# Performance work log

Hardware: AMD Instinct MI355X
Metric: run time of the kernel (lower is better)

## Reference

```python
import jax, jax.numpy as jnp
from jax import lax
import numpy as np

QMAX = 127.0  # int8 symmetric quant range


def setup_inputs() -> dict:
    key = jax.random.key(0)
    k1, k2, k3, k4 = jax.random.split(key, 4)
    B, S, D_in, D_out = 4, 2048, 4096, 4096
    x = jax.random.normal(k1, (B, S, D_in), dtype=jnp.float32)
    # pre-quantized per-channel weights [output_size, input_size]
    weight_q = jax.random.randint(k2, (D_out, D_in), -127, 128, dtype=jnp.int32).astype(jnp.int8)
    weight_scale = (jax.random.uniform(k3, (D_out,), dtype=jnp.float32) + 0.5) * 0.01
    bias = jax.random.normal(k4, (D_out,), dtype=jnp.float32) * 0.02
    return {"x": x, "weight_q": weight_q, "weight_scale": weight_scale, "bias": bias}


def reference(x, weight_q, weight_scale, bias):
    """Dynamic per-token int8 activation quant + int8 matmul + dequant + bias.

    x: [..., D_in] float32; weight_q: [D_out, D_in] int8;
    weight_scale: [D_out]; bias: [D_out]. Returns [..., D_out] float32.
    """
    orig_shape = x.shape
    x2 = x.reshape(-1, orig_shape[-1])  # [T, D_in]
    # dynamic per-token symmetric quantization
    amax = jnp.max(jnp.abs(x2), axis=-1, keepdims=True)  # [T, 1]
    x_scale = jnp.maximum(amax, 1e-8) / QMAX
    x_q = jnp.clip(jnp.round(x2 / x_scale), -128.0, QMAX).astype(jnp.int8)
    acc = lax.dot_general(x_q, weight_q, (((1,), (1,)), ((), ())),
                          preferred_element_type=jnp.int32)  # [T, D_out]
    out = acc.astype(jnp.float32) * x_scale * weight_scale[None, :]
    out = out.reshape(*orig_shape[:-1], out.shape[-1]) + bias
    return out
```

## Files before the change

kernel.cpp:

```cpp
#include <hip/hip_runtime.h>

typedef __attribute__((ext_vector_type(4))) int int4v;

__global__ __launch_bounds__(256) void pack_w_kernel(const int* __restrict__ w32,
                                                     int* __restrict__ w8,
                                                     long n4) {
    long i = (long)blockIdx.x * 256 + threadIdx.x;
    if (i >= n4) return;
    int4v v = ((const int4v*)w32)[i];
    w8[i] = (v[0] & 0xFF) | ((v[1] & 0xFF) << 8) |
            ((v[2] & 0xFF) << 16) | ((v[3] & 0xFF) << 24);
}

template <int NCHUNK>
__global__ __launch_bounds__(256) void quant_kernel(const float* __restrict__ x,
                                                    signed char* __restrict__ xq,
                                                    float* __restrict__ xs,
                                                    int K) {
    const int t = blockIdx.x;
    const int tid = threadIdx.x;
    const float4* row = (const float4*)(x + (size_t)t * K);

    float4 v[NCHUNK];
    float amax = 0.0f;
    #pragma unroll
    for (int i = 0; i < NCHUNK; ++i) {
        float4 f = row[i * 256 + tid];
        v[i] = f;
        amax = fmaxf(amax, fmaxf(fmaxf(fabsf(f.x), fabsf(f.y)),
                                 fmaxf(fabsf(f.z), fabsf(f.w))));
    }
    #pragma unroll
    for (int off = 32; off >= 1; off >>= 1)
        amax = fmaxf(amax, __shfl_xor(amax, off, 64));
    __shared__ float red[4];
    if ((tid & 63) == 0) red[tid >> 6] = amax;
    __syncthreads();
    amax = fmaxf(fmaxf(red[0], red[1]), fmaxf(red[2], red[3]));

    const float scale = fmaxf(amax, 1e-8f) / 127.0f;
    if (tid == 0) xs[t] = scale;
    const float inv = 1.0f / scale;

    int* orow = (int*)(xq + (size_t)t * K);
    #pragma unroll
    for (int i = 0; i < NCHUNK; ++i) {
        float4 f = v[i];
        int q0 = (int)fminf(fmaxf(rintf(f.x * inv), -128.0f), 127.0f);
        int q1 = (int)fminf(fmaxf(rintf(f.y * inv), -128.0f), 127.0f);
        int q2 = (int)fminf(fmaxf(rintf(f.z * inv), -128.0f), 127.0f);
        int q3 = (int)fminf(fmaxf(rintf(f.w * inv), -128.0f), 127.0f);
        orow[i * 256 + tid] =
            (q0 & 0xFF) | ((q1 & 0xFF) << 8) | ((q2 & 0xFF) << 16) | ((q3 & 0xFF) << 24);
    }
}

#define BM 256
#define BN 256
#define BKB 128

#define MFMA_I8 __builtin_amdgcn_mfma_i32_16x16x64_i8

#define BARRIER()                       \
    do {                                \
        __builtin_amdgcn_s_barrier();   \
        asm volatile("" ::: "memory");  \
    } while (0)

#define LGKM0() asm volatile("s_waitcnt lgkmcnt(0)" ::: "memory")
#define VMCNT4() asm volatile("s_waitcnt vmcnt(4)" ::: "memory")

#define STAGE_HALF(GL, LB, ROWOFF, KK)                                        \
    do {                                                                      \
        __builtin_amdgcn_global_load_lds(                                     \
            (const __attribute__((address_space(1))) void*)(                  \
                (GL) + (size_t)(ROWOFF) * K + (KK)),                          \
            (__attribute__((address_space(3))) void*)((LB) + (ROWOFF) * BKB), \
            16, 0, 0);                                                        \
        __builtin_amdgcn_global_load_lds(                                     \
            (const __attribute__((address_space(1))) void*)(                  \
                (GL) + (size_t)((ROWOFF) + 64) * K + (KK)),                   \
            (__attribute__((address_space(3))) void*)(                        \
                (LB) + ((ROWOFF) + 64) * BKB),                                \
            16, 0, 0);                                                        \
    } while (0)

#define LDA4(RP, MOFF)                                                     \
    do {                                                                   \
        af[0][0] = *(const int4v*)((RP) + ((MOFF) + 0) * 2048 + sw0);      \
        af[0][1] = *(const int4v*)((RP) + ((MOFF) + 0) * 2048 + sw1);      \
        af[1][0] = *(const int4v*)((RP) + ((MOFF) + 1) * 2048 + sw0);      \
        af[1][1] = *(const int4v*)((RP) + ((MOFF) + 1) * 2048 + sw1);      \
        af[2][0] = *(const int4v*)((RP) + ((MOFF) + 2) * 2048 + sw0);      \
        af[2][1] = *(const int4v*)((RP) + ((MOFF) + 2) * 2048 + sw1);      \
        af[3][0] = *(const int4v*)((RP) + ((MOFF) + 3) * 2048 + sw0);      \
        af[3][1] = *(const int4v*)((RP) + ((MOFF) + 3) * 2048 + sw1);      \
    } while (0)

#define LDB2M(RP, NB)                                                      \
    do {                                                                   \
        bf[(NB) + 0][0] = *(const int4v*)((RP) + ((NB) + 0) * 2048 + sw0); \
        bf[(NB) + 0][1] = *(const int4v*)((RP) + ((NB) + 0) * 2048 + sw1); \
        bf[(NB) + 1][0] = *(const int4v*)((RP) + ((NB) + 1) * 2048 + sw0); \
        bf[(NB) + 1][1] = *(const int4v*)((RP) + ((NB) + 1) * 2048 + sw1); \
    } while (0)

#define QUAD(MB, NB)                                                          \
    do {                                                                      \
        _Pragma("unroll") for (int m_ = 0; m_ < 4; ++m_) {                    \
            _Pragma("unroll") for (int n_ = 0; n_ < 2; ++n_) {                \
                acc[(MB) + m_][(NB) + n_] = MFMA_I8(                          \
                    af[m_][0], bf[(NB) + n_][0], acc[(MB) + m_][(NB) + n_],   \
                    0, 0, 0);                                                 \
                acc[(MB) + m_][(NB) + n_] = MFMA_I8(                          \
                    af[m_][1], bf[(NB) + n_][1], acc[(MB) + m_][(NB) + n_],   \
                    0, 0, 0);                                                 \
            }                                                                 \
        }                                                                     \
    } while (0)

__global__ __launch_bounds__(512, 2) void gemm_i8_kernel(
    const signed char* __restrict__ A,
    const signed char* __restrict__ B,
    const float* __restrict__ xs,
    const float* __restrict__ wsc,
    const float* __restrict__ bias,
    float* __restrict__ C,
    int M, int N, int K) {
    __shared__ __align__(16) signed char lds[2][2][BM * BKB];

    const int tid = threadIdx.x;
    const int lane = tid & 63;
    const int wv = tid >> 6;
    const int wrow = wv >> 2;
    const int wcol = wv & 3;
    const int fr = lane & 15;
    const int q = lane >> 4;

    const int bm = blockIdx.y * BM;
    const int bn = blockIdx.x * BN;

    const int srow = wv * 8 + (lane >> 3);
    const int scol = ((lane & 7) ^ ((lane >> 3) & 7)) << 4;
    const signed char* gA = A + (size_t)(bm + srow) * K + scol;
    const signed char* gB = B + (size_t)(bn + srow) * K + scol;

    signed char* wA0 = &lds[0][0][0] + wv * 1024;
    signed char* wA1 = &lds[1][0][0] + wv * 1024;
    signed char* wB0 = &lds[0][1][0] + wv * 1024;
    signed char* wB1 = &lds[1][1][0] + wv * 1024;

    const int rowA = (wrow * 128 + fr) * BKB;
    const int rowB = (wcol * 64 + fr) * BKB;
    const int sw0 = ((0 + q) ^ (fr & 7)) << 4;
    const int sw1 = ((4 + q) ^ (fr & 7)) << 4;
    const signed char* rA0 = &lds[0][0][0] + rowA;
    const signed char* rA1 = &lds[1][0][0] + rowA;
    const signed char* rB0 = &lds[0][1][0] + rowB;
    const signed char* rB1 = &lds[1][1][0] + rowB;

    int4v acc[8][4];
    const int4v zero = {0, 0, 0, 0};
    #pragma unroll
    for (int m = 0; m < 8; ++m)
        #pragma unroll
        for (int n = 0; n < 4; ++n) acc[m][n] = zero;
    int4v af[4][2], bf[4][2];

    STAGE_HALF(gA, wA0, 0, 0);
    STAGE_HALF(gA, wA0, 128, 0);
    STAGE_HALF(gB, wB0, 0, 0);
    STAGE_HALF(gB, wB0, 128, 0);
    STAGE_HALF(gB, wB1, 0, (size_t)BKB);
    STAGE_HALF(gB, wB1, 128, (size_t)BKB);
    VMCNT4();
    BARRIER();

    const int NT = K / BKB;
    for (int i = 0; i < NT / 2; ++i) {
        const size_t kk1 = (size_t)(2 * i + 1) * BKB;
        int t2 = 2 * i + 2; if (t2 >= NT) t2 -= NT;
        int t3 = 2 * i + 3; if (t3 >= NT) t3 -= NT;
        const size_t kk2 = (size_t)t2 * BKB;
        const size_t kk3 = (size_t)t3 * BKB;

        LDA4(rA0, 0);
        LDB2M(rB0, 0);
        STAGE_HALF(gA, wA1, 0, kk1);
        BARRIER();
        LGKM0();
        __builtin_amdgcn_s_setprio(1);
        QUAD(0, 0);
        __builtin_amdgcn_s_setprio(0);
        BARRIER();

        LDB2M(rB0, 2);
        STAGE_HALF(gA, wA1, 128, kk1);
        BARRIER();
        LGKM0();
        __builtin_amdgcn_s_setprio(1);
        QUAD(0, 2);
        __builtin_amdgcn_s_setprio(0);
        BARRIER();

        LDA4(rA0, 4);
        STAGE_HALF(gB, wB0, 0, kk2);
        BARRIER();
        LGKM0();
        __builtin_amdgcn_s_setprio(1);
        QUAD(4, 2);
        __builtin_amdgcn_s_setprio(0);
        BARRIER();

        STAGE_HALF(gB, wB0, 128, kk2);
        VMCNT4();
        BARRIER();
        __builtin_amdgcn_s_setprio(1);
        QUAD(4, 0);
        __builtin_amdgcn_s_setprio(0);
        BARRIER();

        LDA4(rA1, 0);
        LDB2M(rB1, 0);
        STAGE_HALF(gA, wA0, 0, kk2);
        BARRIER();
        LGKM0();
        __builtin_amdgcn_s_setprio(1);
        QUAD(0, 0);
        __builtin_amdgcn_s_setprio(0);
        BARRIER();

        LDB2M(rB1, 2);
        STAGE_HALF(gA, wA0, 128, kk2);
        BARRIER();
        LGKM0();
        __builtin_amdgcn_s_setprio(1);
        QUAD(0, 2);
        __builtin_amdgcn_s_setprio(0);
        BARRIER();

        LDA4(rA1, 4);
        STAGE_HALF(gB, wB1, 0, kk3);
        BARRIER();
        LGKM0();
        __builtin_amdgcn_s_setprio(1);
        QUAD(4, 2);
        __builtin_amdgcn_s_setprio(0);
        BARRIER();

        STAGE_HALF(gB, wB1, 128, kk3);
        VMCNT4();
        BARRIER();
        __builtin_amdgcn_s_setprio(1);
        QUAD(4, 0);
        __builtin_amdgcn_s_setprio(0);
        BARRIER();
    }

    asm volatile("s_waitcnt vmcnt(0)" ::: "memory");

    const int cb = bn + wcol * 64;
    float wv4[4], bv4[4];
    #pragma unroll
    for (int n = 0; n < 4; ++n) {
        wv4[n] = wsc[cb + n * 16 + fr];
        bv4[n] = bias[cb + n * 16 + fr];
    }
    #pragma unroll
    for (int m = 0; m < 8; ++m) {
        #pragma unroll
        for (int r = 0; r < 4; ++r) {
            const int row = bm + wrow * 128 + m * 16 + q * 4 + r;
            const float s = xs[row];
            float* crow = C + (size_t)row * N + cb + fr;
            #pragma unroll
            for (int n = 0; n < 4; ++n)
                crow[n * 16] = (float)acc[m][n][r] * s * wv4[n] + bv4[n];
        }
    }
}

extern "C" void kernel_launch(void* const* d_in, const int* in_sizes, int n_in,
                              void* d_out, int out_size, void* d_ws, size_t ws_size,
                              hipStream_t stream) {
    const float* x = (const float*)d_in[0];
    const int* wq32 = (const int*)d_in[1];
    const float* wscale = (const float*)d_in[2];
    const float* bias = (const float*)d_in[3];
    float* out = (float*)d_out;

    const int d_out_dim = in_sizes[2];
    const int d_in_dim = in_sizes[1] / d_out_dim;
    const int T = in_sizes[0] / d_in_dim;

    const size_t wbytes = (size_t)d_out_dim * d_in_dim;
    signed char* w8 = (signed char*)d_ws;
    signed char* xq = (signed char*)d_ws + wbytes;
    float* xscl = (float*)((char*)d_ws + wbytes + (size_t)T * d_in_dim);

    const long n4 = (long)d_out_dim * d_in_dim / 4;
    pack_w_kernel<<<(int)((n4 + 255) / 256), 256, 0, stream>>>(wq32, (int*)w8, n4);

    if (d_in_dim == 4096) {
        quant_kernel<4><<<T, 256, 0, stream>>>(x, xq, xscl, d_in_dim);
    } else {
        quant_kernel<8><<<T, 256, 0, stream>>>(x, xq, xscl, d_in_dim);
    }

    dim3 grid(d_out_dim / BN, T / BM);
    gemm_i8_kernel<<<grid, 512, 0, stream>>>(xq, w8, xscl, wscale, bias, out,
                                             T, d_out_dim, d_in_dim);
}
```

Before: 383.0 us.

## Switch int8 GEMM to 32x32x32 MFMA with reworked fragment loads and epilogue

Replaces the 16x16x64 int8 MFMA with the 32x32x32 variant, so each wave computes its 128x64 tile as 4x2 blocks of 32x32 instead of 8x4 blocks of 16x16. LDS fragment loads, swizzle offsets, the per-phase MFMA schedule and the output row mapping are all rewritten to match the new lane layout. The larger MFMA reduces fragment reloads per FLOP and the number of instructions issued. In exchange, A fragments are now reloaded in every phase, and the epilogue writes wider-strided rows.

```diff
diff --git a/kernel.cpp b/kernel.cpp
--- a/kernel.cpp
+++ b/kernel.cpp
@@ -1,6 +1,7 @@
 #include <hip/hip_runtime.h>
 
 typedef __attribute__((ext_vector_type(4))) int int4v;
+typedef __attribute__((ext_vector_type(16))) int int16v;
 
 __global__ __launch_bounds__(256) void pack_w_kernel(const int* __restrict__ w32,
                                                      int* __restrict__ w8,
@@ -59,7 +60,7 @@
 #define BN 256
 #define BKB 128
 
-#define MFMA_I8 __builtin_amdgcn_mfma_i32_16x16x64_i8
+#define MFMA32 __builtin_amdgcn_mfma_i32_32x32x32_i8
 
 #define BARRIER()                       \
     do {                                \
@@ -85,36 +86,31 @@
             16, 0, 0);                                                        \
     } while (0)
 
-#define LDA4(RP, MOFF)                                                     \
+#define LDA_PAIR(RP, MB, C0, C1)                                           \
     do {                                                                   \
-        af[0][0] = *(const int4v*)((RP) + ((MOFF) + 0) * 2048 + sw0);      \
-        af[0][1] = *(const int4v*)((RP) + ((MOFF) + 0) * 2048 + sw1);      \
-        af[1][0] = *(const int4v*)((RP) + ((MOFF) + 1) * 2048 + sw0);      \
-        af[1][1] = *(const int4v*)((RP) + ((MOFF) + 1) * 2048 + sw1);      \
-        af[2][0] = *(const int4v*)((RP) + ((MOFF) + 2) * 2048 + sw0);      \
-        af[2][1] = *(const int4v*)((RP) + ((MOFF) + 2) * 2048 + sw1);      \
-        af[3][0] = *(const int4v*)((RP) + ((MOFF) + 3) * 2048 + sw0);      \
-        af[3][1] = *(const int4v*)((RP) + ((MOFF) + 3) * 2048 + sw1);      \
-    } while (0)
-
-#define LDB2M(RP, NB)                                                      \
+        af[0][0] = *(const int4v*)((RP) + ((MB) + 0) * 4096 + (C0));       \
+        af[0][1] = *(const int4v*)((RP) + ((MB) + 0) * 4096 + (C1));       \
+        af[1][0] = *(const int4v*)((RP) + ((MB) + 1) * 4096 + (C0));       \
+        af[1][1] = *(const int4v*)((RP) + ((MB) + 1) * 4096 + (C1));       \
+    } while (0)
+
+#define LDB_PAIR(RP, KP, C0, C1)                                           \
     do {                                                                   \
-        bf[(NB) + 0][0] = *(const int4v*)((RP) + ((NB) + 0) * 2048 + sw0); \
-        bf[(NB) + 0][1] = *(const int4v*)((RP) + ((NB) + 0) * 2048 + sw1); \
-        bf[(NB) + 1][0] = *(const int4v*)((RP) + ((NB) + 1) * 2048 + sw0); \
-        bf[(NB) + 1][1] = *(const int4v*)((RP) + ((NB) + 1) * 2048 + sw1); \
-    } while (0)
-
-#define QUAD(MB, NB)                                                          \
+        bf[0][(KP)*2 + 0] = *(const int4v*)((RP) + 0 * 4096 + (C0));       \
+        bf[0][(KP)*2 + 1] = *(const int4v*)((RP) + 0 * 4096 + (C1));       \
+        bf[1][(KP)*2 + 0] = *(const int4v*)((RP) + 1 * 4096 + (C0));       \
+        bf[1][(KP)*2 + 1] = *(const int4v*)((RP) + 1 * 4096 + (C1));       \
+    } while (0)
+
+#define QUAD32(MB, KP)                                                        \
     do {                                                                      \
-        _Pragma("unroll") for (int m_ = 0; m_ < 4; ++m_) {                    \
-            _Pragma("unroll") for (int n_ = 0; n_ < 2; ++n_) {                \
-                acc[(MB) + m_][(NB) + n_] = MFMA_I8(                          \
-                    af[m_][0], bf[(NB) + n_][0], acc[(MB) + m_][(NB) + n_],   \
-                    0, 0, 0);                                                 \
-                acc[(MB) + m_][(NB) + n_] = MFMA_I8(                          \
-                    af[m_][1], bf[(NB) + n_][1], acc[(MB) + m_][(NB) + n_],   \
-                    0, 0, 0);                                                 \
+        _Pragma("unroll") for (int kl_ = 0; kl_ < 2; ++kl_) {                 \
+            _Pragma("unroll") for (int m_ = 0; m_ < 2; ++m_) {                \
+                _Pragma("unroll") for (int n_ = 0; n_ < 2; ++n_) {            \
+                    acc[(MB) + m_][n_] = MFMA32(af[m_][kl_],                  \
+                                                bf[n_][(KP)*2 + kl_],         \
+                                                acc[(MB) + m_][n_], 0, 0, 0); \
+                }                                                             \
             }                                                                 \
         }                                                                     \
     } while (0)
@@ -134,8 +130,8 @@
     const int wv = tid >> 6;
     const int wrow = wv >> 2;
     const int wcol = wv & 3;
-    const int fr = lane & 15;
-    const int q = lane >> 4;
+    const int fr32 = lane & 31;
+    const int kb = lane >> 5;
 
     const int bm = blockIdx.y * BM;
     const int bn = blockIdx.x * BN;
@@ -150,22 +146,27 @@
     signed char* wB0 = &lds[0][1][0] + wv * 1024;
     signed char* wB1 = &lds[1][1][0] + wv * 1024;
 
-    const int rowA = (wrow * 128 + fr) * BKB;
-    const int rowB = (wcol * 64 + fr) * BKB;
-    const int sw0 = ((0 + q) ^ (fr & 7)) << 4;
-    const int sw1 = ((4 + q) ^ (fr & 7)) << 4;
+    const int rowA = (wrow * 128 + fr32) * BKB;
+    const int rowB = (wcol * 64 + fr32) * BKB;
+    const int l7 = lane & 7;
+    const int c0 = ((0 + kb) ^ l7) << 4;
+    const int c1 = ((2 + kb) ^ l7) << 4;
+    const int c2 = ((4 + kb) ^ l7) << 4;
+    const int c3 = ((6 + kb) ^ l7) << 4;
     const signed char* rA0 = &lds[0][0][0] + rowA;
     const signed char* rA1 = &lds[1][0][0] + rowA;
     const signed char* rB0 = &lds[0][1][0] + rowB;
     const signed char* rB1 = &lds[1][1][0] + rowB;
 
-    int4v acc[8][4];
-    const int4v zero = {0, 0, 0, 0};
-    #pragma unroll
-    for (int m = 0; m < 8; ++m)
+    int16v acc[4][2];
+    #pragma unroll
+    for (int m = 0; m < 4; ++m)
         #pragma unroll
-        for (int n = 0; n < 4; ++n) acc[m][n] = zero;
-    int4v af[4][2], bf[4][2];
+        for (int n = 0; n < 2; ++n)
+            #pragma unroll
+            for (int e = 0; e < 16; ++e) acc[m][n][e] = 0;
+    int4v af[2][2];
+    int4v bf[2][4];
 
     STAGE_HALF(gA, wA0, 0, 0);
     STAGE_HALF(gA, wA0, 128, 0);
@@ -184,75 +185,81 @@
         const size_t kk2 = (size_t)t2 * BKB;
         const size_t kk3 = (size_t)t3 * BKB;
 
-        LDA4(rA0, 0);
-        LDB2M(rB0, 0);
+        LDB_PAIR(rB0, 0, c0, c1);
+        LDA_PAIR(rA0, 0, c0, c1);
         STAGE_HALF(gA, wA1, 0, kk1);
         BARRIER();
         LGKM0();
         __builtin_amdgcn_s_setprio(1);
-        QUAD(0, 0);
-        __builtin_amdgcn_s_setprio(0);
-        BARRIER();
-
-        LDB2M(rB0, 2);
+        QUAD32(0, 0);
+        __builtin_amdgcn_s_setprio(0);
+        BARRIER();
+
+        LDB_PAIR(rB0, 1, c2, c3);
+        LDA_PAIR(rA0, 0, c2, c3);
         STAGE_HALF(gA, wA1, 128, kk1);
         BARRIER();
         LGKM0();
         __builtin_amdgcn_s_setprio(1);
-        QUAD(0, 2);
-        __builtin_amdgcn_s_setprio(0);
-        BARRIER();
-
-        LDA4(rA0, 4);
+        QUAD32(0, 1);
+        __builtin_amdgcn_s_setprio(0);
+        BARRIER();
+
+        LDA_PAIR(rA0, 2, c0, c1);
         STAGE_HALF(gB, wB0, 0, kk2);
         BARRIER();
         LGKM0();
         __builtin_amdgcn_s_setprio(1);
-        QUAD(4, 2);
-        __builtin_amdgcn_s_setprio(0);
-        BARRIER();
-
+        QUAD32(2, 0);
+        __builtin_amdgcn_s_setprio(0);
+        BARRIER();
+
+        LDA_PAIR(rA0, 2, c2, c3);
         STAGE_HALF(gB, wB0, 128, kk2);
         VMCNT4();
         BARRIER();
-        __builtin_amdgcn_s_setprio(1);
-        QUAD(4, 0);
-        __builtin_amdgcn_s_setprio(0);
-        BARRIER();
-
-        LDA4(rA1, 0);
-        LDB2M(rB1, 0);
+        LGKM0();
+        __builtin_amdgcn_s_setprio(1);
+        QUAD32(2, 1);
+        __builtin_amdgcn_s_setprio(0);
+        BARRIER();
+
+        LDB_PAIR(rB1, 0, c0, c1);
+        LDA_PAIR(rA1, 0, c0, c1);
         STAGE_HALF(gA, wA0, 0, kk2);
         BARRIER();
         LGKM0();
         __builtin_amdgcn_s_setprio(1);
-        QUAD(0, 0);
-        __builtin_amdgcn_s_setprio(0);
-        BARRIER();
-
-        LDB2M(rB1, 2);
+        QUAD32(0, 0);
+        __builtin_amdgcn_s_setprio(0);
+        BARRIER();
+
+        LDB_PAIR(rB1, 1, c2, c3);
+        LDA_PAIR(rA1, 0, c2, c3);
         STAGE_HALF(gA, wA0, 128, kk2);
         BARRIER();
         LGKM0();
         __builtin_amdgcn_s_setprio(1);
-        QUAD(0, 2);
-        __builtin_amdgcn_s_setprio(0);
-        BARRIER();
-
-        LDA4(rA1, 4);
+        QUAD32(0, 1);
+        __builtin_amdgcn_s_setprio(0);
+        BARRIER();
+
+        LDA_PAIR(rA1, 2, c0, c1);
         STAGE_HALF(gB, wB1, 0, kk3);
         BARRIER();
         LGKM0();
         __builtin_amdgcn_s_setprio(1);
-        QUAD(4, 2);
-        __builtin_amdgcn_s_setprio(0);
-        BARRIER();
-
+        QUAD32(2, 0);
+        __builtin_amdgcn_s_setprio(0);
+        BARRIER();
+
+        LDA_PAIR(rA1, 2, c2, c3);
         STAGE_HALF(gB, wB1, 128, kk3);
         VMCNT4();
         BARRIER();
-        __builtin_amdgcn_s_setprio(1);
-        QUAD(4, 0);
+        LGKM0();
+        __builtin_amdgcn_s_setprio(1);
+        QUAD32(2, 1);
         __builtin_amdgcn_s_setprio(0);
         BARRIER();
     }
@@ -260,22 +267,21 @@
     asm volatile("s_waitcnt vmcnt(0)" ::: "memory");
 
     const int cb = bn + wcol * 64;
-    float wv4[4], bv4[4];
-    #pragma unroll
-    for (int n = 0; n < 4; ++n) {
-        wv4[n] = wsc[cb + n * 16 + fr];
-        bv4[n] = bias[cb + n * 16 + fr];
-    }
-    #pragma unroll
-    for (int m = 0; m < 8; ++m) {
+    float wv2[2], bv2[2];
+    #pragma unroll
+    for (int n = 0; n < 2; ++n) {
+        wv2[n] = wsc[cb + n * 32 + fr32];
+        bv2[n] = bias[cb + n * 32 + fr32];
+    }
+    #pragma unroll
+    for (int m = 0; m < 4; ++m) {
         #pragma unroll
-        for (int r = 0; r < 4; ++r) {
-            const int row = bm + wrow * 128 + m * 16 + q * 4 + r;
+        for (int r = 0; r < 16; ++r) {
+            const int row = bm + wrow * 128 + m * 32 + (r & 3) + 8 * (r >> 2) + 4 * kb;
             const float s = xs[row];
-            float* crow = C + (size_t)row * N + cb + fr;
-            #pragma unroll
-            for (int n = 0; n < 4; ++n)
-                crow[n * 16] = (float)acc[m][n][r] * s * wv4[n] + bv4[n];
+            float* crow = C + (size_t)row * N + cb + fr32;
+            crow[0]  = (float)acc[m][0][r] * s * wv2[0] + bv2[0];
+            crow[32] = (float)acc[m][1][r] * s * wv2[1] + bv2[1];
         }
     }
 }
```

Measured after the change: 399.4 us. 4.3% more time.

## Reorder GEMM phases by k-sub-slice to shrink A-fragment registers

Applied to the files above, without the earlier changes.

Restructures the 8-phase main loop so each phase covers all four N sub-tiles for one k half-slice, instead of two N sub-tiles over both k halves. The A fragment buffer shrinks from 4x2 to 4 vectors, which lowers VGPR pressure under the 2-waves-per-SIMD launch bound. In exchange, A fragments are now read from LDS twice as often (once per k half), and the fourth phase gains an extra LDS load and wait. LDS traffic per iteration goes up while register use goes down.

```diff
diff --git a/kernel.cpp b/kernel.cpp
--- a/kernel.cpp
+++ b/kernel.cpp
@@ -85,36 +85,28 @@
             16, 0, 0);                                                        \
     } while (0)
 
-#define LDA4(RP, MOFF)                                                     \
+#define LDA_KS(RP, MOFF, SW)                                               \
     do {                                                                   \
-        af[0][0] = *(const int4v*)((RP) + ((MOFF) + 0) * 2048 + sw0);      \
-        af[0][1] = *(const int4v*)((RP) + ((MOFF) + 0) * 2048 + sw1);      \
-        af[1][0] = *(const int4v*)((RP) + ((MOFF) + 1) * 2048 + sw0);      \
-        af[1][1] = *(const int4v*)((RP) + ((MOFF) + 1) * 2048 + sw1);      \
-        af[2][0] = *(const int4v*)((RP) + ((MOFF) + 2) * 2048 + sw0);      \
-        af[2][1] = *(const int4v*)((RP) + ((MOFF) + 2) * 2048 + sw1);      \
-        af[3][0] = *(const int4v*)((RP) + ((MOFF) + 3) * 2048 + sw0);      \
-        af[3][1] = *(const int4v*)((RP) + ((MOFF) + 3) * 2048 + sw1);      \
-    } while (0)
-
-#define LDB2M(RP, NB)                                                      \
+        af[0] = *(const int4v*)((RP) + ((MOFF) + 0) * 2048 + (SW));        \
+        af[1] = *(const int4v*)((RP) + ((MOFF) + 1) * 2048 + (SW));        \
+        af[2] = *(const int4v*)((RP) + ((MOFF) + 2) * 2048 + (SW));        \
+        af[3] = *(const int4v*)((RP) + ((MOFF) + 3) * 2048 + (SW));        \
+    } while (0)
+
+#define LDB_KS(RP, KS, SW)                                                 \
     do {                                                                   \
-        bf[(NB) + 0][0] = *(const int4v*)((RP) + ((NB) + 0) * 2048 + sw0); \
-        bf[(NB) + 0][1] = *(const int4v*)((RP) + ((NB) + 0) * 2048 + sw1); \
-        bf[(NB) + 1][0] = *(const int4v*)((RP) + ((NB) + 1) * 2048 + sw0); \
-        bf[(NB) + 1][1] = *(const int4v*)((RP) + ((NB) + 1) * 2048 + sw1); \
-    } while (0)
-
-#define QUAD(MB, NB)                                                          \
+        bf[0][(KS)] = *(const int4v*)((RP) + 0 * 2048 + (SW));             \
+        bf[1][(KS)] = *(const int4v*)((RP) + 1 * 2048 + (SW));             \
+        bf[2][(KS)] = *(const int4v*)((RP) + 2 * 2048 + (SW));             \
+        bf[3][(KS)] = *(const int4v*)((RP) + 3 * 2048 + (SW));             \
+    } while (0)
+
+#define PH_MFMA(MB, KS)                                                       \
     do {                                                                      \
         _Pragma("unroll") for (int m_ = 0; m_ < 4; ++m_) {                    \
-            _Pragma("unroll") for (int n_ = 0; n_ < 2; ++n_) {                \
-                acc[(MB) + m_][(NB) + n_] = MFMA_I8(                          \
-                    af[m_][0], bf[(NB) + n_][0], acc[(MB) + m_][(NB) + n_],   \
-                    0, 0, 0);                                                 \
-                acc[(MB) + m_][(NB) + n_] = MFMA_I8(                          \
-                    af[m_][1], bf[(NB) + n_][1], acc[(MB) + m_][(NB) + n_],   \
-                    0, 0, 0);                                                 \
+            _Pragma("unroll") for (int n_ = 0; n_ < 4; ++n_) {                \
+                acc[(MB) + m_][n_] = MFMA_I8(af[m_], bf[n_][(KS)],            \
+                                             acc[(MB) + m_][n_], 0, 0, 0);    \
             }                                                                 \
         }                                                                     \
     } while (0)
@@ -165,7 +157,8 @@
     for (int m = 0; m < 8; ++m)
         #pragma unroll
         for (int n = 0; n < 4; ++n) acc[m][n] = zero;
-    int4v af[4][2], bf[4][2];
+    int4v af[4];
+    int4v bf[4][2];
 
     STAGE_HALF(gA, wA0, 0, 0);
     STAGE_HALF(gA, wA0, 128, 0);
@@ -184,75 +177,81 @@
         const size_t kk2 = (size_t)t2 * BKB;
         const size_t kk3 = (size_t)t3 * BKB;
 
-        LDA4(rA0, 0);
-        LDB2M(rB0, 0);
+        LDA_KS(rA0, 0, sw0);
+        LDB_KS(rB0, 0, sw0);
         STAGE_HALF(gA, wA1, 0, kk1);
         BARRIER();
         LGKM0();
         __builtin_amdgcn_s_setprio(1);
-        QUAD(0, 0);
-        __builtin_amdgcn_s_setprio(0);
-        BARRIER();
-
-        LDB2M(rB0, 2);
+        PH_MFMA(0, 0);
+        __builtin_amdgcn_s_setprio(0);
+        BARRIER();
+
+        LDA_KS(rA0, 0, sw1);
+        LDB_KS(rB0, 1, sw1);
         STAGE_HALF(gA, wA1, 128, kk1);
         BARRIER();
         LGKM0();
         __builtin_amdgcn_s_setprio(1);
-        QUAD(0, 2);
-        __builtin_amdgcn_s_setprio(0);
-        BARRIER();
-
-        LDA4(rA0, 4);
+        PH_MFMA(0, 1);
+        __builtin_amdgcn_s_setprio(0);
+        BARRIER();
+
+        LDA_KS(rA0, 4, sw0);
         STAGE_HALF(gB, wB0, 0, kk2);
         BARRIER();
         LGKM0();
         __builtin_amdgcn_s_setprio(1);
-        QUAD(4, 2);
-        __builtin_amdgcn_s_setprio(0);
-        BARRIER();
-
+        PH_MFMA(4, 0);
+        __builtin_amdgcn_s_setprio(0);
+        BARRIER();
+
+        LDA_KS(rA0, 4, sw1);
         STAGE_HALF(gB, wB0, 128, kk2);
         VMCNT4();
         BARRIER();
-        __builtin_amdgcn_s_setprio(1);
-        QUAD(4, 0);
-        __builtin_amdgcn_s_setprio(0);
-        BARRIER();
-
-        LDA4(rA1, 0);
-        LDB2M(rB1, 0);
+        LGKM0();
+        __builtin_amdgcn_s_setprio(1);
+        PH_MFMA(4, 1);
+        __builtin_amdgcn_s_setprio(0);
+        BARRIER();
+
+        LDA_KS(rA1, 0, sw0);
+        LDB_KS(rB1, 0, sw0);
         STAGE_HALF(gA, wA0, 0, kk2);
         BARRIER();
         LGKM0();
         __builtin_amdgcn_s_setprio(1);
-        QUAD(0, 0);
-        __builtin_amdgcn_s_setprio(0);
-        BARRIER();
-
-        LDB2M(rB1, 2);
+        PH_MFMA(0, 0);
+        __builtin_amdgcn_s_setprio(0);
+        BARRIER();
+
+        LDA_KS(rA1, 0, sw1);
+        LDB_KS(rB1, 1, sw1);
         STAGE_HALF(gA, wA0, 128, kk2);
         BARRIER();
         LGKM0();
         __builtin_amdgcn_s_setprio(1);
-        QUAD(0, 2);
-        __builtin_amdgcn_s_setprio(0);
-        BARRIER();
-
-        LDA4(rA1, 4);
+        PH_MFMA(0, 1);
+        __builtin_amdgcn_s_setprio(0);
+        BARRIER();
+
+        LDA_KS(rA1, 4, sw0);
         STAGE_HALF(gB, wB1, 0, kk3);
         BARRIER();
         LGKM0();
         __builtin_amdgcn_s_setprio(1);
-        QUAD(4, 2);
-        __builtin_amdgcn_s_setprio(0);
-        BARRIER();
-
+        PH_MFMA(4, 0);
+        __builtin_amdgcn_s_setprio(0);
+        BARRIER();
+
+        LDA_KS(rA1, 4, sw1);
         STAGE_HALF(gB, wB1, 128, kk3);
         VMCNT4();
         BARRIER();
-        __builtin_amdgcn_s_setprio(1);
-        QUAD(4, 0);
+        LGKM0();
+        __builtin_amdgcn_s_setprio(1);
+        PH_MFMA(4, 1);
         __builtin_amdgcn_s_setprio(0);
         BARRIER();
     }
```

Result: no change. 379.8 us (-0.8%).
